# Optimization experiments

Measured on AMD Instinct MI355X. Metric: run time of the kernel, lower is better.

## Reference

```python
import jax, jax.numpy as jnp
import numpy as np

D_MODEL = 1024
D_Q = 1024
D_V = 1024


def setup_inputs() -> dict:
    key = jax.random.key(0)
    k0, k1, k2, k3 = jax.random.split(key, 4)
    embedding_word = jax.random.normal(k0, (4, 2048, D_MODEL), dtype=jnp.float32)
    # nn.Linear weights are [out, in]; we store transposed [in, out] for x @ W
    s = 1.0 / np.sqrt(D_MODEL)
    w_q = jax.random.uniform(k1, (D_MODEL, D_Q), jnp.float32, -s, s)
    w_k = jax.random.uniform(k2, (D_MODEL, D_Q), jnp.float32, -s, s)
    w_v = jax.random.uniform(k3, (D_MODEL, D_V), jnp.float32, -s, s)
    return {"embedding_word": embedding_word, "w_q": w_q, "w_k": w_k, "w_v": w_v}


def reference(embedding_word, w_q, w_k, w_v):
    # q,k: [B,T,d_q]; v: [B,T,d_v]
    q = embedding_word @ w_q
    k = embedding_word @ w_k
    v = embedding_word @ w_v
    scores = jnp.einsum("btd,bsd->bts", q, k)  # [B,T,T]
    T = scores.shape[-1]
    causal = jnp.tril(jnp.ones((T, T), dtype=bool))  # True = keep
    masked = jnp.where(causal, scores, -jnp.inf)
    weights = jax.nn.softmax(masked / jnp.sqrt(jnp.float32(D_Q)), axis=-1)
    return jnp.einsum("bts,bsv->btv", weights, v)
```

## Files before the change

kernel.cpp:

```cpp
#include <hip/hip_runtime.h>
#include <cstdint>

typedef __bf16 bf16_t;
typedef __attribute__((ext_vector_type(8))) __bf16 bf16x8;
typedef __attribute__((ext_vector_type(4))) __bf16 bf16x4;
typedef __attribute__((ext_vector_type(4))) float f32x4;

#define AS1 __attribute__((address_space(1)))
#define AS3 __attribute__((address_space(3)))

__device__ __forceinline__ void load_lds16(const void* g, void* l) {
  __builtin_amdgcn_global_load_lds((const AS1 void*)g, (AS3 void*)l, 16, 0, 0);
}

template <typename OutT>
__global__ __launch_bounds__(256)
void gemm_nt(const bf16_t* __restrict__ A, const bf16_t* __restrict__ B,
             OutT* __restrict__ C, int K, int lda, int ldb, int ldc,
             long sA, long sB, long sC, int causalSkip, int kLimit)
{
  const int bm = blockIdx.y, bn = blockIdx.x;
  if (causalSkip && bn > bm) return;
  A += (long)blockIdx.z * sA;
  B += (long)blockIdx.z * sB;
  C += (long)blockIdx.z * sC;
  const int m0 = bm * 128, n0 = bn * 128;
  const int Keff = kLimit ? ((K < (bm + 1) * 128) ? K : (bm + 1) * 128) : K;

  __shared__ bf16_t As[128 * 32];
  __shared__ bf16_t Bs[128 * 32];

  const int tid = threadIdx.x;
  const int wave = tid >> 6, lane = tid & 63;
  const int lm = lane & 15, q = lane >> 4;
  const int wm = (wave >> 1) * 64, wn = (wave & 1) * 64;

  const int c1 = tid, c2 = tid + 256;
  const bf16_t* Ag1 = A + (long)(m0 + (c1 >> 2)) * lda + ((c1 & 3) << 3);
  const bf16_t* Ag2 = A + (long)(m0 + (c2 >> 2)) * lda + ((c2 & 3) << 3);
  const bf16_t* Bg1 = B + (long)(n0 + (c1 >> 2)) * ldb + ((c1 & 3) << 3);
  const bf16_t* Bg2 = B + (long)(n0 + (c2 >> 2)) * ldb + ((c2 & 3) << 3);
  bf16_t* sA1 = As + wave * 512;
  bf16_t* sA2 = As + 2048 + wave * 512;
  bf16_t* sB1 = Bs + wave * 512;
  bf16_t* sB2 = Bs + 2048 + wave * 512;

  f32x4 acc[4][4] = {};

  for (int k0 = 0; k0 < Keff; k0 += 32) {
    load_lds16(Ag1 + k0, sA1);
    load_lds16(Ag2 + k0, sA2);
    load_lds16(Bg1 + k0, sB1);
    load_lds16(Bg2 + k0, sB2);
    __syncthreads();
    bf16x8 aF[4], bF[4];
#pragma unroll
    for (int i = 0; i < 4; i++)
      aF[i] = *(const bf16x8*)&As[(wm + i * 16 + lm) * 32 + q * 8];
#pragma unroll
    for (int j = 0; j < 4; j++)
      bF[j] = *(const bf16x8*)&Bs[(wn + j * 16 + lm) * 32 + q * 8];
#pragma unroll
    for (int i = 0; i < 4; i++)
#pragma unroll
      for (int j = 0; j < 4; j++)
        acc[i][j] = __builtin_amdgcn_mfma_f32_16x16x32_bf16(aF[i], bF[j], acc[i][j], 0, 0, 0);
    __syncthreads();
  }

#pragma unroll
  for (int i = 0; i < 4; i++) {
    const int row = m0 + wm + i * 16 + q * 4;
#pragma unroll
    for (int j = 0; j < 4; j++) {
      const int col = n0 + wn + j * 16 + lm;
#pragma unroll
      for (int r = 0; r < 4; r++)
        C[(long)(row + r) * ldc + col] = (OutT)acc[i][j][r];
    }
  }
}

__global__ void cvt_f32_bf16(const float* __restrict__ in, bf16_t* __restrict__ out, int n4)
{
  const int i = blockIdx.x * blockDim.x + threadIdx.x;
  if (i >= n4) return;
  const float4 f = ((const float4*)in)[i];
  bf16x4 o = {(bf16_t)f.x, (bf16_t)f.y, (bf16_t)f.z, (bf16_t)f.w};
  ((bf16x4*)out)[i] = o;
}

__global__ void cvt_transpose_w(const float* __restrict__ wq, const float* __restrict__ wk,
                                const float* __restrict__ wv, bf16_t* __restrict__ WT)
{
  const float* W = (blockIdx.z == 0) ? wq : (blockIdx.z == 1) ? wk : wv;
  bf16_t* O = WT + (long)blockIdx.z * 1024 * 1024;
  __shared__ float tile[32][33];
  const int x = blockIdx.x * 32 + threadIdx.x;
  const int y = blockIdx.y * 32 + threadIdx.y;
  tile[threadIdx.y][threadIdx.x] = W[(long)y * 1024 + x];
  __syncthreads();
  const int ox = blockIdx.x * 32 + threadIdx.y;
  const int oy = blockIdx.y * 32 + threadIdx.x;
  O[(long)ox * 1024 + oy] = (bf16_t)tile[threadIdx.x][threadIdx.y];
}

__global__ __launch_bounds__(256)
void softmax_causal(bf16_t* __restrict__ S)
{
  const int row = blockIdx.x;
  const int t = row & 2047;
  bf16_t* Sr = S + (long)row * 2048;
  const int base = threadIdx.x * 8;

  uint4 u = *(const uint4*)(Sr + base);
  const unsigned short* up = (const unsigned short*)&u;
  float v[8];
  float m = -3.0e38f;
#pragma unroll
  for (int j = 0; j < 8; j++) {
    const float x = __uint_as_float(((unsigned)up[j]) << 16);
    v[j] = (base + j <= t) ? x : -3.0e38f;
    m = fmaxf(m, v[j]);
  }
#pragma unroll
  for (int off = 32; off > 0; off >>= 1) m = fmaxf(m, __shfl_xor(m, off));
  __shared__ float redm[4], redl[4];
  const int wave = threadIdx.x >> 6, lane = threadIdx.x & 63;
  if (lane == 0) redm[wave] = m;
  __syncthreads();
  m = fmaxf(fmaxf(redm[0], redm[1]), fmaxf(redm[2], redm[3]));

  float p[8], l = 0.f;
#pragma unroll
  for (int j = 0; j < 8; j++) {
    p[j] = (base + j <= t) ? __expf((v[j] - m) * 0.03125f) : 0.f;
    l += p[j];
  }
#pragma unroll
  for (int off = 32; off > 0; off >>= 1) l += __shfl_xor(l, off);
  if (lane == 0) redl[wave] = l;
  __syncthreads();
  l = (redl[0] + redl[1]) + (redl[2] + redl[3]);
  const float rl = 1.0f / l;

  uint4 w;
  unsigned* wp = (unsigned*)&w;
#pragma unroll
  for (int h = 0; h < 4; h++) {
    bf16_t a = (bf16_t)(p[2 * h] * rl);
    bf16_t b = (bf16_t)(p[2 * h + 1] * rl);
    wp[h] = (unsigned)__builtin_bit_cast(unsigned short, a) |
            ((unsigned)__builtin_bit_cast(unsigned short, b) << 16);
  }
  *(uint4*)(Sr + base) = w;
}

extern "C" void kernel_launch(void* const* d_in, const int* in_sizes, int n_in,
                              void* d_out, int out_size, void* d_ws, size_t ws_size,
                              hipStream_t stream)
{
  const float* X  = (const float*)d_in[0];
  const float* Wq = (const float*)d_in[1];
  const float* Wk = (const float*)d_in[2];
  const float* Wv = (const float*)d_in[3];
  float* out = (float*)d_out;

  char* p = (char*)d_ws;
  bf16_t* QK = (bf16_t*)p;  p += (size_t)8192 * 2048 * 2;
  bf16_t* VT = (bf16_t*)p;  p += (size_t)1024 * 8192 * 2;
  bf16_t* WT = (bf16_t*)p;  p += (size_t)3072 * 1024 * 2;
  bf16_t* Xb = (bf16_t*)p;
  bf16_t* S  = (bf16_t*)p;

  cvt_f32_bf16<<<8192, 256, 0, stream>>>(X, Xb, 8388608 / 4);
  cvt_transpose_w<<<dim3(32, 32, 3), dim3(32, 32), 0, stream>>>(Wq, Wk, Wv, WT);
  gemm_nt<bf16_t><<<dim3(16, 64), 256, 0, stream>>>(
      Xb, WT, QK, 1024, 1024, 1024, 2048, 0, 0, 0, 0, 0);
  gemm_nt<bf16_t><<<dim3(64, 8), 256, 0, stream>>>(
      WT + (long)2048 * 1024, Xb, VT, 1024, 1024, 1024, 8192, 0, 0, 0, 0, 0);
  gemm_nt<bf16_t><<<dim3(16, 16, 4), 256, 0, stream>>>(
      QK, QK + 1024, S, 1024, 2048, 2048, 2048,
      (long)2048 * 2048, (long)2048 * 2048, (long)2048 * 2048, 1, 0);
  softmax_causal<<<8192, 256, 0, stream>>>(S);
  gemm_nt<float><<<dim3(8, 16, 4), 256, 0, stream>>>(
      S, VT, out, 2048, 2048, 8192, 1024,
      (long)2048 * 2048, 2048, (long)2048 * 1024, 0, 1);
}
```

Measured before the change: 307.6 us.

## Double GEMM K-tile to 64 with k-chunk-major LDS layout and reversed causal scheduling

Raises the GEMM K step from 32 to 64, halving the number of barrier pairs per tile. The LDS layout changes so each 16-byte chunk column is stored contiguously by row, which should reduce bank conflicts on fragment reads. For the kLimit PV GEMM, row blocks are issued in reverse so the longest causal tiles start first, improving load balance. LDS use doubles to 32KB per block, which may lower occupancy.

```diff
diff --git a/kernel.cpp b/kernel.cpp
--- a/kernel.cpp
+++ b/kernel.cpp
@@ -9,68 +9,70 @@
 #define AS1 __attribute__((address_space(1)))
 #define AS3 __attribute__((address_space(3)))
 
-__device__ __forceinline__ void load_lds16(const void* g, void* l) {
-  __builtin_amdgcn_global_load_lds((const AS1 void*)g, (AS3 void*)l, 16, 0, 0);
-}
-
 template <typename OutT>
 __global__ __launch_bounds__(256)
 void gemm_nt(const bf16_t* __restrict__ A, const bf16_t* __restrict__ B,
              OutT* __restrict__ C, int K, int lda, int ldb, int ldc,
              long sA, long sB, long sC, int causalSkip, int kLimit)
 {
-  const int bm = blockIdx.y, bn = blockIdx.x;
+  int bm = blockIdx.y;
+  const int bn = blockIdx.x;
+  if (kLimit) bm = gridDim.y - 1 - bm;
   if (causalSkip && bn > bm) return;
   A += (long)blockIdx.z * sA;
   B += (long)blockIdx.z * sB;
   C += (long)blockIdx.z * sC;
   const int m0 = bm * 128, n0 = bn * 128;
-  const int Keff = kLimit ? ((K < (bm + 1) * 128) ? K : (bm + 1) * 128) : K;
+  int Keff = K;
+  if (kLimit) { const int kl = (bm + 1) * 128; if (kl < Keff) Keff = kl; }
 
-  __shared__ bf16_t As[128 * 32];
-  __shared__ bf16_t Bs[128 * 32];
+  __shared__ bf16_t As[128 * 64];
+  __shared__ bf16_t Bs[128 * 64];
 
   const int tid = threadIdx.x;
   const int wave = tid >> 6, lane = tid & 63;
-  const int lm = lane & 15, q = lane >> 4;
+  const int lm = lane & 15, qd = lane >> 4;
   const int wm = (wave >> 1) * 64, wn = (wave & 1) * 64;
 
-  const int c1 = tid, c2 = tid + 256;
-  const bf16_t* Ag1 = A + (long)(m0 + (c1 >> 2)) * lda + ((c1 & 3) << 3);
-  const bf16_t* Ag2 = A + (long)(m0 + (c2 >> 2)) * lda + ((c2 & 3) << 3);
-  const bf16_t* Bg1 = B + (long)(n0 + (c1 >> 2)) * ldb + ((c1 & 3) << 3);
-  const bf16_t* Bg2 = B + (long)(n0 + (c2 >> 2)) * ldb + ((c2 & 3) << 3);
-  bf16_t* sA1 = As + wave * 512;
-  bf16_t* sA2 = As + 2048 + wave * 512;
-  bf16_t* sB1 = Bs + wave * 512;
-  bf16_t* sB2 = Bs + 2048 + wave * 512;
+  const int rl = wave * 64 + lane;
+  const int srow = rl & 127, shi = rl >> 7;
+  const bf16_t* Abase = A + (long)(m0 + srow) * lda + shi * 8;
+  const bf16_t* Bbase = B + (long)(n0 + srow) * ldb + shi * 8;
+  bf16_t* AsW = As + wave * 512;
+  bf16_t* BsW = Bs + wave * 512;
 
   f32x4 acc[4][4] = {};
 
-  for (int k0 = 0; k0 < Keff; k0 += 32) {
-    load_lds16(Ag1 + k0, sA1);
-    load_lds16(Ag2 + k0, sA2);
-    load_lds16(Bg1 + k0, sB1);
-    load_lds16(Bg2 + k0, sB2);
+  for (int k0 = 0; k0 < Keff; k0 += 64) {
+#pragma unroll
+    for (int i = 0; i < 4; i++) {
+      __builtin_amdgcn_global_load_lds((const AS1 void*)(Abase + k0 + i * 16),
+                                       (AS3 void*)(AsW + i * 2048), 16, 0, 0);
+      __builtin_amdgcn_global_load_lds((const AS1 void*)(Bbase + k0 + i * 16),
+                                       (AS3 void*)(BsW + i * 2048), 16, 0, 0);
+    }
     __syncthreads();
-    bf16x8 aF[4], bF[4];
 #pragma unroll
-    for (int i = 0; i < 4; i++)
-      aF[i] = *(const bf16x8*)&As[(wm + i * 16 + lm) * 32 + q * 8];
+    for (int s = 0; s < 2; s++) {
+      bf16x8 aF[4], bF[4];
 #pragma unroll
-    for (int j = 0; j < 4; j++)
-      bF[j] = *(const bf16x8*)&Bs[(wn + j * 16 + lm) * 32 + q * 8];
-#pragma unroll
-    for (int i = 0; i < 4; i++)
+      for (int i = 0; i < 4; i++)
+        aF[i] = *(const bf16x8*)&As[(s * 4 + qd) * 1024 + (wm + i * 16 + lm) * 8];
 #pragma unroll
       for (int j = 0; j < 4; j++)
-        acc[i][j] = __builtin_amdgcn_mfma_f32_16x16x32_bf16(aF[i], bF[j], acc[i][j], 0, 0, 0);
+        bF[j] = *(const bf16x8*)&Bs[(s * 4 + qd) * 1024 + (wn + j * 16 + lm) * 8];
+#pragma unroll
+      for (int i = 0; i < 4; i++)
+#pragma unroll
+        for (int j = 0; j < 4; j++)
+          acc[i][j] = __builtin_amdgcn_mfma_f32_16x16x32_bf16(aF[i], bF[j], acc[i][j], 0, 0, 0);
+    }
     __syncthreads();
   }
 
 #pragma unroll
   for (int i = 0; i < 4; i++) {
-    const int row = m0 + wm + i * 16 + q * 4;
+    const int row = m0 + wm + i * 16 + qd * 4;
 #pragma unroll
     for (int j = 0; j < 4; j++) {
       const int col = n0 + wn + j * 16 + lm;
```

Result: slower. 395.2 us (+28.5%).
